# Kernel optimization log

Measured on AMD Instinct MI355X. Metric: run time of the kernel, lower is better.

The kernel has to match this reference:

```python
import jax, jax.numpy as jnp
import numpy as np
import math

D = 256        # input_size == d_k == d_v (per the module: d_k = input_size)
H = 4          # n_heads
MAX_LEN = 800  # PositionalEncoding max_len
NEG = float(-(2**32) + 1)
LN_EPS = 1e-5


def _make_pe():
    pe = np.zeros((MAX_LEN, D), dtype=np.float32)
    pos = np.arange(MAX_LEN, dtype=np.float32)[:, None]
    div = np.exp(np.arange(0, D, 2, dtype=np.float32) * -(math.log(10000.0) / D))
    pe[:, 0::2] = np.sin(pos * div)
    pe[:, 1::2] = np.cos(pos * div)
    return jnp.asarray(pe)


def setup_inputs() -> dict:
    key = jax.random.key(0)
    ks = jax.random.split(key, 12)
    B, L = 32, 512

    def xavier(k, shape):
        fan_in, fan_out = shape[0], shape[1]
        std = math.sqrt(2.0 / (fan_in + fan_out))
        return jax.random.normal(k, shape, dtype=jnp.float32) * std

    return {
        "Q": jax.random.normal(ks[0], (B, L, D), dtype=jnp.float32),
        "K": jax.random.normal(ks[1], (B, L, D), dtype=jnp.float32),
        "V": jax.random.normal(ks[2], (B, L, D), dtype=jnp.float32),
        "mask": jax.random.randint(ks[3], (B, L), 0, 2).astype(jnp.bool_),
        "pe": _make_pe(),
        "W_q": xavier(ks[4], (D, H * D)),
        "W_k": xavier(ks[5], (D, H * D)),
        "W_v": xavier(ks[6], (D, H * D)),
        "W_o": xavier(ks[7], (H * D, D)),
        "w1": xavier(ks[8], (D, D)),
        "b1": jnp.zeros((D,), dtype=jnp.float32),
        "w2": xavier(ks[9], (D, D)),
        "b2": jnp.zeros((D,), dtype=jnp.float32),
        "gamma": jnp.ones((D,), dtype=jnp.float32),
        "beta": jnp.zeros((D,), dtype=jnp.float32),
    }


def _layer_norm(x, gamma, beta):
    mu = jnp.mean(x, axis=-1, keepdims=True)
    var = jnp.mean(jnp.square(x - mu), axis=-1, keepdims=True)
    return (x - mu) * jax.lax.rsqrt(var + LN_EPS) * gamma + beta


def _mha(Q, K, V, mask, W_q, W_k, W_v, W_o):
    B, Lq, _ = Q.shape
    Lk = K.shape[1]

    def split_heads(X, W, L):
        # (B, L, D) @ (D, H*D) -> (B*H, L, D)
        return (X @ W).reshape(B, L, H, D).transpose(0, 2, 1, 3).reshape(B * H, L, D)

    Qh = split_heads(Q, W_q, Lq)
    Kh = split_heads(K, W_k, Lk)
    Vh = split_heads(V, W_v, Lk)

    scale = D ** 0.5 + 1e-6
    scores = jnp.einsum('bqd,bkd->bqk', Qh, Kh) / scale  # (B*H, Lq, Lk)

    pad = jnp.broadcast_to(mask[:, None, :], (B, H, Lq)).reshape(B * H, Lq)
    pad_mask = jnp.broadcast_to(pad[:, :, None], (B * H, Lq, Lk))
    causal = jnp.triu(jnp.ones((Lq, Lk), dtype=jnp.bool_), k=1)
    full_mask = causal[None] | pad_mask
    scores = jnp.where(full_mask, NEG, scores)

    att = jax.nn.softmax(scores, axis=-1)
    Vatt = jnp.einsum('bqk,bkd->bqd', att, Vh)  # (B*H, Lq, D)
    Vatt = Vatt.reshape(B, H, Lq, D).transpose(0, 2, 1, 3).reshape(B, Lq, H * D)
    return Vatt @ W_o


def reference(Q, K, V, mask, pe, W_q, W_k, W_v, W_o, w1, b1, w2, b2, gamma, beta):
    Lq, Lk, Lv = Q.shape[1], K.shape[1], V.shape[1]
    Qp = Q + pe[None, :Lq]
    Kp = K + pe[None, :Lk]
    Vp = V + pe[None, :Lv]

    Vatt = _mha(Qp, Kp, Vp, mask, W_q, W_k, W_v, W_o)
    X = _layer_norm(Qp + Vatt, gamma, beta)
    ffn = jax.nn.relu(X @ w1.T + b1) @ w2.T + b2
    return _layer_norm(ffn + X, gamma, beta)
```

## Files before the change

kernel.cpp:

```cpp
#include <hip/hip_runtime.h>
#include <stdint.h>

#define SEQ   512
#define DM    256
#define NB    32
#define NH    4
#define HD    (NH * DM)
#define PE_MASK (SEQ * DM - 1)
#define NEGV  (-4294967295.0f)

typedef __attribute__((ext_vector_type(8))) short short8;
typedef __attribute__((ext_vector_type(4))) float f32x4;

#if defined(__has_builtin)
#if __has_builtin(__builtin_amdgcn_global_load_lds)
#define HAS_ASYNC 1
#endif
#endif
#ifndef HAS_ASYNC
#define HAS_ASYNC 0
#endif

__device__ __forceinline__ float b2f(unsigned short u) {
    return __uint_as_float(((uint32_t)u) << 16);
}
__device__ __forceinline__ unsigned short f2b(float f) {
    uint32_t u = __float_as_uint(f);
    u += 0x7fffu + ((u >> 16) & 1u);
    return (unsigned short)(u >> 16);
}
__device__ __forceinline__ float fast_exp2(float x) {
    float r;
    asm("v_exp_f32 %0, %1" : "=v"(r) : "v"(x));
    return r;
}

__device__ __forceinline__ int swzb(int b) {
    return b ^ (((b >> 7) & 7) << 4);
}

__global__ __launch_bounds__(256) void prep_all(
    const unsigned char* __restrict__ mask_raw, int* __restrict__ maskc,
    const float* __restrict__ Wq, const float* __restrict__ Wk,
    const float* __restrict__ Wv, unsigned short* __restrict__ WqT,
    const float* __restrict__ Wo, unsigned short* __restrict__ WoT,
    const float* __restrict__ w1, const float* __restrict__ w2,
    unsigned short* __restrict__ o1, unsigned short* __restrict__ o2,
    const float* __restrict__ Q, const float* __restrict__ K,
    const float* __restrict__ V, const float* __restrict__ pe,
    unsigned short* __restrict__ Qp, unsigned short* __restrict__ Kp,
    unsigned short* __restrict__ Vp)
{
    __shared__ unsigned short tile[32][33];
    __shared__ int enc[2];
    const int blk = blockIdx.x;
    const int tid = threadIdx.x;

    if (blk < 64) {
        if (tid == 0) { enc[0] = 0; enc[1] = 0; }
        __syncthreads();
        if (tid < 255 && mask_raw[tid * 4 + 1]) atomicOr(&enc[0], 1);
        if (tid < 128 && ((const int*)mask_raw)[tid * 2 + 1]) atomicOr(&enc[1], 1);
        __syncthreads();
        int i = blk * 256 + tid;
        int v;
        if (enc[0])      v = (mask_raw[i] != 0);
        else if (enc[1]) v = (((const int*)mask_raw)[i] != 0);
        else             v = ((((const int*)mask_raw)[i * 2] |
                              ((const int*)mask_raw)[i * 2 + 1]) != 0);
        maskc[i] = v;
    } else if (blk < 832) {
        int t = blk - 64;
        int x = t & 31, y = (t >> 5) & 7, zz = t >> 8;
        const float* in = (zz == 0) ? Wq : (zz == 1) ? Wk : Wv;
        unsigned short* op = WqT + (long)zz * 262144;
        int r0 = y * 32, c0 = x * 32;
        int i = tid >> 3, j = (tid & 7) * 4;
        float4 v = *reinterpret_cast<const float4*>(in + (long)(r0 + i) * HD + c0 + j);
        tile[i][j + 0] = f2b(v.x); tile[i][j + 1] = f2b(v.y);
        tile[i][j + 2] = f2b(v.z); tile[i][j + 3] = f2b(v.w);
        __syncthreads();
        ushort4 w;
        w.x = tile[j + 0][i]; w.y = tile[j + 1][i];
        w.z = tile[j + 2][i]; w.w = tile[j + 3][i];
        *reinterpret_cast<ushort4*>(op + (long)(c0 + i) * DM + r0 + j) = w;
    } else if (blk < 1088) {
        int t = blk - 832;
        int x = t & 7, y = t >> 3;
        int r0 = y * 32, c0 = x * 32;
        int i = tid >> 3, j = (tid & 7) * 4;
        float4 v = *reinterpret_cast<const float4*>(Wo + (long)(r0 + i) * DM + c0 + j);
        tile[i][j + 0] = f2b(v.x); tile[i][j + 1] = f2b(v.y);
        tile[i][j + 2] = f2b(v.z); tile[i][j + 3] = f2b(v.w);
        __syncthreads();
        ushort4 w;
        w.x = tile[j + 0][i]; w.y = tile[j + 1][i];
        w.z = tile[j + 2][i]; w.w = tile[j + 3][i];
        *reinterpret_cast<ushort4*>(WoT + (long)(c0 + i) * HD + r0 + j) = w;
    } else if (blk < 1216) {
        int t = blk - 1088;
        const float* in = (t < 64) ? w1 : w2;
        unsigned short* out = (t < 64) ? o1 : o2;
        long i = (long)((t & 63) * 256 + tid) * 4;
        float4 x = *reinterpret_cast<const float4*>(in + i);
        ushort4 o;
        o.x = f2b(x.x); o.y = f2b(x.y); o.z = f2b(x.z); o.w = f2b(x.w);
        *reinterpret_cast<ushort4*>(out + i) = o;
    } else {
        int t = blk - 1216;
        int seg = t >> 12;
        const float* X = (seg == 0) ? Q : (seg == 1) ? K : V;
        unsigned short* O = (seg == 0) ? Qp : (seg == 1) ? Kp : Vp;
        long i = (long)((t & 4095) * 256 + tid) * 4;
        float4 x = *reinterpret_cast<const float4*>(X + i);
        float4 p = *reinterpret_cast<const float4*>(pe + (i & PE_MASK));
        ushort4 o;
        o.x = f2b(x.x + p.x); o.y = f2b(x.y + p.y);
        o.z = f2b(x.z + p.z); o.w = f2b(x.w + p.w);
        *reinterpret_cast<ushort4*>(O + i) = o;
    }
}

__global__ __launch_bounds__(256) void tv_kernel(
    const unsigned short* __restrict__ Vh, unsigned short* __restrict__ VhT,
    float* __restrict__ part, int nbl)
{
    __shared__ unsigned short tile[32][33];
    const int blk = blockIdx.x;
    const int tid = threadIdx.x;
    const int nT = nbl * NH * 128;

    if (blk < nT) {
        int x = blk & 7, y = (blk >> 3) & 15, zz = blk >> 7;
        int b = zz / NH, hh = zz % NH;
        const unsigned short* ip = Vh + (long)b * SEQ * HD + (long)hh * DM;
        unsigned short* op = VhT + (long)b * SEQ * HD + (long)hh * SEQ * DM;
        int r0 = y * 32, c0 = x * 32;
        int i = tid >> 3, j = (tid & 7) * 4;
        ushort4 v = *reinterpret_cast<const ushort4*>(ip + (long)(r0 + i) * HD + c0 + j);
        tile[i][j + 0] = v.x; tile[i][j + 1] = v.y;
        tile[i][j + 2] = v.z; tile[i][j + 3] = v.w;
        __syncthreads();
        ushort4 w;
        w.x = tile[j + 0][i]; w.y = tile[j + 1][i];
        w.z = tile[j + 2][i]; w.w = tile[j + 3][i];
        *reinterpret_cast<ushort4*>(op + (long)(c0 + i) * SEQ + r0 + j) = w;
    } else {
        int t = blk - nT;
        int bl = t >> 3, seg = t & 7;
        const unsigned short* p = Vh + (long)bl * SEQ * HD + (long)seg * 64 * HD;
        int c = tid * 4;
        float s0 = 0.f, s1 = 0.f, s2 = 0.f, s3 = 0.f;
        for (int l = 0; l < 64; ++l) {
            ushort4 v = *reinterpret_cast<const ushort4*>(p + (long)l * HD + c);
            s0 += b2f(v.x); s1 += b2f(v.y); s2 += b2f(v.z); s3 += b2f(v.w);
        }
        float4 o = {s0, s1, s2, s3};
        *reinterpret_cast<float4*>(part + (long)(bl * 8 + seg) * HD + c) = o;
    }
}

template<bool BIAS, bool RELU, bool OUTBF16>
__global__ __launch_bounds__(256) void gemm_bt(
    const unsigned short* __restrict__ A, int lda,
    const unsigned short* __restrict__ B, int ldb,
    void* __restrict__ Cv, int ldc,
    const float* __restrict__ bias, float scale, int K, int Hdiv,
    long sAb, long sAh, long sAz,
    long sBb, long sBh, long sBz,
    long sCb, long sCh, long sCz)
{
    const int m0 = blockIdx.y * 128;
    const int n0 = blockIdx.x * 128;
    int z  = blockIdx.z;
    int bb = z / Hdiv, hh = z % Hdiv;
    const unsigned short* Ab = A + bb * sAb + hh * sAh + (long)z * sAz;
    const unsigned short* Bb = B + bb * sBb + hh * sBh + (long)z * sBz;
    long coff = bb * sCb + hh * sCh + (long)z * sCz;
    const float scl = (z == 0) ? scale : 1.0f;

    __shared__ unsigned short As[2][128 * 32];
    __shared__ unsigned short Bs[2][128 * 32];

    const int tid  = threadIdx.x;
    const int lane = tid & 63;
    const int wave = tid >> 6;
    const int wm   = (wave >> 1) * 64;
    const int wn   = (wave & 1) * 64;
    const int lm   = lane & 15;
    const int kq   = (lane >> 4) * 8;

    f32x4 acc[4][4] = {};

    auto stage = [&](int b, int k0) {
#pragma unroll
        for (int it = 0; it < 2; ++it) {
            int id = tid + it * 256;
#if HAS_ASYNC
            int U  = swzb(id * 16);
            int r  = U >> 6;
            int c8 = ((U >> 4) & 3) * 8;
            const unsigned short* gA = Ab + (long)(m0 + r) * lda + k0 + c8;
            const unsigned short* gB = Bb + (long)(n0 + r) * ldb + k0 + c8;
            unsigned short* lA = &As[b][(size_t)(it * 256 + wave * 64) * 8];
            unsigned short* lB = &Bs[b][(size_t)(it * 256 + wave * 64) * 8];
            __builtin_amdgcn_global_load_lds(
                (const __attribute__((address_space(1))) void*)gA,
                (__attribute__((address_space(3))) void*)lA, 16, 0, 0);
            __builtin_amdgcn_global_load_lds(
                (const __attribute__((address_space(1))) void*)gB,
                (__attribute__((address_space(3))) void*)lB, 16, 0, 0);
#else
            int r  = id >> 2;
            int c8 = (id & 3) * 8;
            const unsigned short* gA = Ab + (long)(m0 + r) * lda + k0 + c8;
            const unsigned short* gB = Bb + (long)(n0 + r) * ldb + k0 + c8;
            *reinterpret_cast<uint4*>((char*)As[b] + swzb(id * 16)) =
                *reinterpret_cast<const uint4*>(gA);
            *reinterpret_cast<uint4*>((char*)Bs[b] + swzb(id * 16)) =
                *reinterpret_cast<const uint4*>(gB);
#endif
        }
    };

    stage(0, 0);
    __syncthreads();
    const int nk = K >> 5;
    for (int kk = 0; kk < nk; ++kk) {
        const int cur = kk & 1;
        if (kk + 1 < nk)
            stage(cur ^ 1, (kk + 1) * 32);

        short8 af[4], bfr[4];
#pragma unroll
        for (int i = 0; i < 4; ++i)
            af[i] = *reinterpret_cast<const short8*>(
                (const char*)As[cur] + swzb((wm + i * 16 + lm) * 64 + kq * 2));
#pragma unroll
        for (int j = 0; j < 4; ++j)
            bfr[j] = *reinterpret_cast<const short8*>(
                (const char*)Bs[cur] + swzb((wn + j * 16 + lm) * 64 + kq * 2));
#pragma unroll
        for (int i = 0; i < 4; ++i)
#pragma unroll
            for (int j = 0; j < 4; ++j)
                acc[i][j] = __builtin_amdgcn_mfma_f32_16x16x32_bf16(af[i], bfr[j], acc[i][j], 0, 0, 0);
        __syncthreads();
    }

#pragma unroll
    for (int j = 0; j < 4; ++j) {
        int col  = n0 + wn + j * 16 + lm;
        float bv = 0.f;
        if (BIAS) bv = bias[col];
#pragma unroll
        for (int i = 0; i < 4; ++i) {
#pragma unroll
            for (int r = 0; r < 4; ++r) {
                int row = m0 + wm + i * 16 + (lane >> 4) * 4 + r;
                float v = acc[i][j][r] * scl + bv;
                if (RELU) v = fmaxf(v, 0.f);
                long idx = coff + (long)row * ldc + col;
                if (OUTBF16) reinterpret_cast<unsigned short*>(Cv)[idx] = f2b(v);
                else         reinterpret_cast<float*>(Cv)[idx] = v;
            }
        }
    }
}

__device__ __forceinline__ void stage_k32(
    unsigned short* __restrict__ buf, const unsigned short* __restrict__ Ak,
    int kc, int qt, int tid, int wave)
{
    for (int it = 0; it <= qt; ++it) {
        int id = tid + it * 256;
#if HAS_ASYNC
        int U = swzb(id * 16);
        const unsigned short* g = Ak + (long)(U >> 6) * HD + kc * 32 + ((U >> 4) & 3) * 8;
        unsigned short* l = buf + (size_t)(it * 256 + wave * 64) * 8;
        __builtin_amdgcn_global_load_lds(
            (const __attribute__((address_space(1))) void*)g,
            (__attribute__((address_space(3))) void*)l, 16, 0, 0);
#else
        const unsigned short* g = Ak + (long)(id >> 2) * HD + kc * 32 + (id & 3) * 8;
        *reinterpret_cast<uint4*>((char*)buf + swzb(id * 16)) =
            *reinterpret_cast<const uint4*>(g);
#endif
    }
}

__device__ __forceinline__ void stage_v64(
    unsigned short* __restrict__ buf, const unsigned short* __restrict__ Av,
    int c64, int tid, int wave)
{
#pragma unroll
    for (int it = 0; it < 8; ++it) {
        int id = tid + it * 256;
#if HAS_ASYNC
        int U = swzb(id * 16);
        const unsigned short* g = Av + (long)(U >> 7) * SEQ + c64 * 64 + ((U >> 4) & 7) * 8;
        unsigned short* l = buf + (size_t)(it * 256 + wave * 64) * 8;
        __builtin_amdgcn_global_load_lds(
            (const __attribute__((address_space(1))) void*)g,
            (__attribute__((address_space(3))) void*)l, 16, 0, 0);
#else
        const unsigned short* g = Av + (long)(id >> 3) * SEQ + c64 * 64 + (id & 7) * 8;
        *reinterpret_cast<uint4*>((char*)buf + swzb(id * 16)) =
            *reinterpret_cast<const uint4*>(g);
#endif
    }
}

__global__ __launch_bounds__(256, 2) void flash_attn(
    const unsigned short* __restrict__ Qh,
    const unsigned short* __restrict__ Kh,
    const unsigned short* __restrict__ VhT,
    const float* __restrict__ part,
    unsigned short* __restrict__ Vatt,
    const int* __restrict__ maskc, int bh0, int nbh)
{
    const int tid  = threadIdx.x;
    const int lane = tid & 63;
    const int wave = tid >> 6;
    const int lm   = lane & 15;
    const int qg   = lane >> 4;
    const int kq   = qg * 8;

    const int L = blockIdx.x;
    int z, qt;
    if ((nbh & 7) == 0) {
        int x = L & 7, m = L >> 3;
        int mq = m & 7;
        qt = (mq & 1) ? (7 - (mq >> 1)) : (mq >> 1);
        z  = x + 8 * (m >> 3);
    } else {
        z = L % nbh; qt = L / nbh;
    }
    const int b_l = z >> 2, h = z & 3;
    const int m0  = qt * 64;
    const int wq0 = m0 + wave * 16;
    const long qkbase = (long)b_l * SEQ * HD + (long)h * DM;
    const unsigned short* Aq = Qh + qkbase;
    const unsigned short* Ak = Kh + qkbase;
    const unsigned short* Av = VhT + (long)b_l * SEQ * HD + (long)h * SEQ * DM;
    unsigned short* Ov = Vatt + qkbase;
    const int bglob = (bh0 + z) >> 2;

    __shared__ unsigned short Ks[2 * SEQ * 32];
    __shared__ __align__(16) unsigned short Pw[4][16][40];

    f32x4 S[32] = {};
    const int NT = (m0 >> 4) + wave + 1;

    stage_k32(Ks, Ak, 0, qt, tid, wave);
    __syncthreads();
    for (int kc = 0; kc < 8; ++kc) {
        unsigned short* cur = (kc & 1) ? (Ks + SEQ * 32) : Ks;
        unsigned short* nxt = (kc & 1) ? Ks : (Ks + SEQ * 32);
        short8 qf = *reinterpret_cast<const short8*>(
            Aq + (long)(wq0 + lm) * HD + kc * 32 + kq);
        if (kc < 7) {
            stage_k32(nxt, Ak, kc + 1, qt, tid, wave);
        } else {
            stage_v64(Ks, Av, 0, tid, wave);
        }
        __builtin_amdgcn_s_setprio(1);
#pragma unroll
        for (int nt = 0; nt < 32; ++nt) {
            if (nt < NT) {
                int row = nt * 16 + lm;
                short8 bf = *reinterpret_cast<const short8*>(
                    (const char*)cur + swzb(row * 64 + qg * 16));
                S[nt] = __builtin_amdgcn_mfma_f32_16x16x32_bf16(qf, bf, S[nt], 0, 0, 0);
            }
        }
        __builtin_amdgcn_s_setprio(0);
        __syncthreads();
    }

    int   qrow[4];
    bool  rowm[4];
    float mx[4], sm[4];
#pragma unroll
    for (int r = 0; r < 4; ++r) {
        int q = wq0 + qg * 4 + r;
        qrow[r] = q;
        rowm[r] = maskc[bglob * SEQ + q] != 0;
        mx[r] = -3.4e38f;
    }
#pragma unroll
    for (int nt = 0; nt < 32; ++nt) {
        int k = nt * 16 + lm;
#pragma unroll
        for (int r = 0; r < 4; ++r) {
            float v = S[nt][r];
            if (k > qrow[r]) v = NEGV;
            S[nt][r] = v;
            mx[r] = fmaxf(mx[r], v);
        }
    }
#pragma unroll
    for (int r = 0; r < 4; ++r) {
#pragma unroll
        for (int off = 8; off >= 1; off >>= 1)
            mx[r] = fmaxf(mx[r], __shfl_xor(mx[r], off));
        sm[r] = 0.f;
    }
    uint32_t pk[32][2];
#pragma unroll
    for (int nt = 0; nt < 32; ++nt) {
        float e0 = fast_exp2(S[nt][0] - mx[0]);
        float e1 = fast_exp2(S[nt][1] - mx[1]);
        float e2 = fast_exp2(S[nt][2] - mx[2]);
        float e3 = fast_exp2(S[nt][3] - mx[3]);
        sm[0] += e0; sm[1] += e1; sm[2] += e2; sm[3] += e3;
        pk[nt][0] = (uint32_t)f2b(e0) | ((uint32_t)f2b(e1) << 16);
        pk[nt][1] = (uint32_t)f2b(e2) | ((uint32_t)f2b(e3) << 16);
    }
#pragma unroll
    for (int r = 0; r < 4; ++r) {
#pragma unroll
        for (int off = 8; off >= 1; off >>= 1)
            sm[r] += __shfl_xor(sm[r], off);
        sm[r] = 1.0f / sm[r];
    }

    unsigned short* Vb0 = Ks;
    unsigned short* Vb1 = Ks + 16384;
    const int NC = qt + 1;
    f32x4 O[16] = {};
#pragma unroll
    for (int c64 = 0; c64 < 8; ++c64) {
        if (c64 < NC) {
            unsigned short* Vcur = (c64 & 1) ? Vb1 : Vb0;
            __syncthreads();
            if (c64 + 1 < NC) {
                unsigned short* Vnext = (c64 & 1) ? Vb0 : Vb1;
                stage_v64(Vnext, Av, c64 + 1, tid, wave);
            }
#pragma unroll
            for (int t = 0; t < 2; ++t) {
#pragma unroll
                for (int tt = 0; tt < 2; ++tt) {
                    int nt = c64 * 4 + t * 2 + tt;
#pragma unroll
                    for (int r = 0; r < 4; ++r)
                        Pw[wave][qg * 4 + r][tt * 16 + lm] =
                            (unsigned short)(pk[nt][r >> 1] >> ((r & 1) * 16));
                }
                short8 pf = *reinterpret_cast<const short8*>(&Pw[wave][lm][kq]);
                __builtin_amdgcn_s_setprio(1);
#pragma unroll
                for (int nt2 = 0; nt2 < 16; ++nt2) {
                    int row = nt2 * 16 + lm;
                    short8 vf = *reinterpret_cast<const short8*>(
                        (const char*)Vcur + swzb(row * 128 + t * 64 + qg * 16));
                    O[nt2] = __builtin_amdgcn_mfma_f32_16x16x32_bf16(pf, vf, O[nt2], 0, 0, 0);
                }
                __builtin_amdgcn_s_setprio(0);
            }
        }
    }

    const float* pb = part + (long)(b_l * 8) * HD + h * DM + lm;
    float vmf[16];
#pragma unroll
    for (int nt2 = 0; nt2 < 16; ++nt2) {
        float s = 0.f;
#pragma unroll
        for (int seg = 0; seg < 8; ++seg)
            s += pb[(long)seg * HD + nt2 * 16];
        vmf[nt2] = s * (1.0f / SEQ);
    }
#pragma unroll
    for (int nt2 = 0; nt2 < 16; ++nt2) {
#pragma unroll
        for (int r = 0; r < 4; ++r) {
            int l = wq0 + qg * 4 + r;
            float val = rowm[r] ? vmf[nt2] : O[nt2][r] * sm[r];
            Ov[(long)l * HD + nt2 * 16 + lm] = f2b(val);
        }
    }
}

__global__ __launch_bounds__(256) void ln1_kernel(
    const unsigned short* __restrict__ AttO, const float* __restrict__ Q,
    const float* __restrict__ pe,
    const float* __restrict__ gamma, const float* __restrict__ beta,
    float* __restrict__ outf, unsigned short* __restrict__ outb)
{
    int row  = blockIdx.x * 4 + (threadIdx.x >> 6);
    int lane = threadIdx.x & 63;
    long base = (long)row * DM + lane * 4;
    ushort4 a = *reinterpret_cast<const ushort4*>(AttO + base);
    float4 qv = *reinterpret_cast<const float4*>(Q + base);
    float4 pv = *reinterpret_cast<const float4*>(pe + (base & PE_MASK));
    float x[4] = {b2f(a.x) + qv.x + pv.x, b2f(a.y) + qv.y + pv.y,
                  b2f(a.z) + qv.z + pv.z, b2f(a.w) + qv.w + pv.w};
    float s = x[0] + x[1] + x[2] + x[3];
#pragma unroll
    for (int off = 32; off > 0; off >>= 1) s += __shfl_xor(s, off);
    float mu = s * (1.0f / DM);
    float vs = 0.f;
#pragma unroll
    for (int t = 0; t < 4; ++t) { float d = x[t] - mu; vs += d * d; }
#pragma unroll
    for (int off = 32; off > 0; off >>= 1) vs += __shfl_xor(vs, off);
    float inv = rsqrtf(vs * (1.0f / DM) + 1e-5f);
    int d0 = lane * 4;
    float4 g = *reinterpret_cast<const float4*>(gamma + d0);
    float4 bt = *reinterpret_cast<const float4*>(beta + d0);
    float4 o;
    o.x = (x[0] - mu) * inv * g.x + bt.x;
    o.y = (x[1] - mu) * inv * g.y + bt.y;
    o.z = (x[2] - mu) * inv * g.z + bt.z;
    o.w = (x[3] - mu) * inv * g.w + bt.w;
    *reinterpret_cast<float4*>(outf + base) = o;
    ushort4 ob;
    ob.x = f2b(o.x); ob.y = f2b(o.y); ob.z = f2b(o.z); ob.w = f2b(o.w);
    *reinterpret_cast<ushort4*>(outb + base) = ob;
}

__global__ __launch_bounds__(256) void ln2_kernel(
    const float* __restrict__ F, const float* __restrict__ X,
    const float* __restrict__ gamma, const float* __restrict__ beta,
    float* __restrict__ out)
{
    int row  = blockIdx.x * 4 + (threadIdx.x >> 6);
    int lane = threadIdx.x & 63;
    long base = (long)row * DM + lane * 4;
    float4 a = *reinterpret_cast<const float4*>(F + base);
    float4 c = *reinterpret_cast<const float4*>(X + base);
    float x[4] = {a.x + c.x, a.y + c.y, a.z + c.z, a.w + c.w};
    float s = x[0] + x[1] + x[2] + x[3];
#pragma unroll
    for (int off = 32; off > 0; off >>= 1) s += __shfl_xor(s, off);
    float mu = s * (1.0f / DM);
    float vs = 0.f;
#pragma unroll
    for (int t = 0; t < 4; ++t) { float d = x[t] - mu; vs += d * d; }
#pragma unroll
    for (int off = 32; off > 0; off >>= 1) vs += __shfl_xor(vs, off);
    float inv = rsqrtf(vs * (1.0f / DM) + 1e-5f);
    int d0 = lane * 4;
    float4 g = *reinterpret_cast<const float4*>(gamma + d0);
    float4 bt = *reinterpret_cast<const float4*>(beta + d0);
    float4 o;
    o.x = (x[0] - mu) * inv * g.x + bt.x;
    o.y = (x[1] - mu) * inv * g.y + bt.y;
    o.z = (x[2] - mu) * inv * g.z + bt.z;
    o.w = (x[3] - mu) * inv * g.w + bt.w;
    *reinterpret_cast<float4*>(out + base) = o;
}

extern "C" void kernel_launch(void* const* d_in, const int* in_sizes, int n_in,
                              void* d_out, int out_size, void* d_ws, size_t ws_size,
                              hipStream_t stream)
{
    const float* Q  = (const float*)d_in[0];
    const float* Ki = (const float*)d_in[1];
    const float* Vi = (const float*)d_in[2];
    const unsigned char* mask_raw = (const unsigned char*)d_in[3];
    const float* pe = (const float*)d_in[4];
    const float* Wq = (const float*)d_in[5];
    const float* Wk = (const float*)d_in[6];
    const float* Wv = (const float*)d_in[7];
    const float* Wo = (const float*)d_in[8];
    const float* w1 = (const float*)d_in[9];
    const float* b1 = (const float*)d_in[10];
    const float* w2 = (const float*)d_in[11];
    const float* b2 = (const float*)d_in[12];
    const float* gamma = (const float*)d_in[13];
    const float* beta  = (const float*)d_in[14];
    float* out = (float*)d_out;

    const size_t MiB = 1048576;
    char* ws = (char*)d_ws;

    int CB = 1;
    for (int cb = 32; cb >= 1; cb >>= 1) {
        size_t scr_sz = (size_t)(5 * cb) * MiB + (size_t)cb * 32768;
        if (scr_sz < 24 * MiB) scr_sz = 24 * MiB;
        if ((59 * MiB + scr_sz) <= ws_size) { CB = cb; break; }
    }
    const int NCH = NB / CB;

    unsigned short* WqT  = (unsigned short*)(ws);
    unsigned short* WkT  = WqT + 262144;
    unsigned short* WvT  = WkT + 262144;
    unsigned short* WoT  = WvT + 262144;
    unsigned short* w1b  = (unsigned short*)(ws + 2 * MiB);
    unsigned short* w2b  = w1b + 65536;
    int*            maskc = (int*)(ws + 2 * MiB + 262144);
    unsigned short* Qp   = (unsigned short*)(ws + 3 * MiB);
    unsigned short* Kp   = (unsigned short*)(ws + 11 * MiB);
    unsigned short* Vp   = (unsigned short*)(ws + 19 * MiB);
    unsigned short* AttO = (unsigned short*)(ws + 27 * MiB);
    unsigned short* Xb   = (unsigned short*)(ws + 35 * MiB);
    float*          Xf   = (float*)(ws + 43 * MiB);
    char*           scr  = ws + 59 * MiB;
    unsigned short* Qh   = (unsigned short*)(scr);
    unsigned short* Kh   = (unsigned short*)(scr + (size_t)CB * MiB);
    unsigned short* Vh   = (unsigned short*)(scr + (size_t)2 * CB * MiB);
    unsigned short* VhT  = (unsigned short*)(scr + (size_t)3 * CB * MiB);
    unsigned short* Vatt = (unsigned short*)(scr + (size_t)4 * CB * MiB);
    float*          part = (float*)(scr + (size_t)5 * CB * MiB);
    unsigned short* H1   = (unsigned short*)(scr);
    float*          Ff   = (float*)(scr + 8 * MiB);

    const float SCALE_Q = (float)((1.0 / (16.0 + 1e-6)) * 1.4426950408889634);
    const long CROWS = (long)CB * SEQ;
    const long CBELT = (long)CB * MiB / 2;

    prep_all<<<13504, 256, 0, stream>>>(
        mask_raw, maskc, Wq, Wk, Wv, WqT, Wo, WoT,
        w1, w2, w1b, w2b, Q, Ki, Vi, pe, Qp, Kp, Vp);

    for (int c = 0; c < NCH; ++c) {
        const long r0   = (long)c * CROWS;
        const int  bh0  = c * CB * NH;
        const int  gy   = (int)(CROWS / 128);
        const int  nbh  = CB * NH;

        gemm_bt<false, false, true><<<dim3(8, gy, 3), 256, 0, stream>>>(
            Qp + r0 * DM, DM, WqT, DM, Qh, HD, nullptr, SCALE_Q, DM,
            1, 4194304, 0, 0, 262144, 0, 0, CBELT, 0, 0);

        tv_kernel<<<CB * NH * 128 + CB * 8, 256, 0, stream>>>(
            Vh, VhT, part, CB);

        flash_attn<<<dim3(8 * nbh, 1, 1), 256, 0, stream>>>(
            Qh, Kh, VhT, part, Vatt, maskc, bh0, nbh);

        gemm_bt<false, false, true><<<dim3(2, gy, 1), 256, 0, stream>>>(
            Vatt, HD, WoT, HD, AttO + r0 * DM, DM, nullptr, 1.f, HD,
            1, 0,0,0, 0,0,0, 0,0,0);
    }

    ln1_kernel<<<4096, 256, 0, stream>>>(AttO, Q, pe, gamma, beta, Xf, Xb);

    gemm_bt<true, true, true><<<dim3(2, 128, 1), 256, 0, stream>>>(
        Xb, DM, w1b, DM, H1, DM, b1, 1.f, DM, 1, 0,0,0, 0,0,0, 0,0,0);
    gemm_bt<true, false, false><<<dim3(2, 128, 1), 256, 0, stream>>>(
        H1, DM, w2b, DM, Ff, DM, b2, 1.f, DM, 1, 0,0,0, 0,0,0, 0,0,0);

    ln2_kernel<<<4096, 256, 0, stream>>>(Ff, Xf, gamma, beta, out);
}
```

Before: 324.7 us.

## Fuse output-projection and FFN2 GEMMs with residual layernorm epilogues

Adds a gemm_ln kernel in which each block computes a full 64x256 output row tile and applies the residual add, optional positional encoding and bias, and layernorm in the epilogue through an LDS staging tile. It replaces the W_o GEMM plus ln1 and the second FFN GEMM plus ln2, removing the intermediate AttO and Ff buffers and two extra launches. In exchange each block must own the whole 256-wide row, so fewer blocks run (for example 256 for FFN2), which lowers parallelism and uses a large LDS tile that may reduce occupancy.

```diff
diff --git a/kernel.cpp b/kernel.cpp
--- a/kernel.cpp
+++ b/kernel.cpp
@@ -268,6 +268,155 @@
     }
 }
 
+template<bool ADDPE, bool BIAS, bool OUTB16>
+__global__ __launch_bounds__(256) void gemm_ln(
+    const unsigned short* __restrict__ A, int lda,
+    const unsigned short* __restrict__ B, int ldb,
+    const float* __restrict__ bias,
+    const float* __restrict__ Rf, const float* __restrict__ pe,
+    const float* __restrict__ gamma, const float* __restrict__ beta,
+    float* __restrict__ outf, unsigned short* __restrict__ outb,
+    int K, long row0)
+{
+    const int m0 = blockIdx.x * 64;
+
+    __shared__ __align__(16) float Xt[64][260];
+    unsigned short* Sh = reinterpret_cast<unsigned short*>(&Xt[0][0]);
+    unsigned short* AsP[2] = { Sh, Sh + 2048 };
+    unsigned short* BsP[2] = { Sh + 4096, Sh + 4096 + 8192 };
+
+    const int tid  = threadIdx.x;
+    const int lane = tid & 63;
+    const int wave = tid >> 6;
+    const int wm   = (wave >> 1) * 32;
+    const int wn   = (wave & 1) * 128;
+    const int lm   = lane & 15;
+    const int qg   = lane >> 4;
+    const int kq   = qg * 8;
+
+    f32x4 acc[2][8] = {};
+
+    auto stage = [&](int b, int k0) {
+        {
+            int id = tid;
+#if HAS_ASYNC
+            int U  = swzb(id * 16);
+            int r  = U >> 6;
+            int c8 = ((U >> 4) & 3) * 8;
+            const unsigned short* gA = A + (long)(m0 + r) * lda + k0 + c8;
+            unsigned short* lA = AsP[b] + (size_t)(wave * 64) * 8;
+            __builtin_amdgcn_global_load_lds(
+                (const __attribute__((address_space(1))) void*)gA,
+                (__attribute__((address_space(3))) void*)lA, 16, 0, 0);
+#else
+            int r  = id >> 2;
+            int c8 = (id & 3) * 8;
+            const unsigned short* gA = A + (long)(m0 + r) * lda + k0 + c8;
+            *reinterpret_cast<uint4*>((char*)AsP[b] + swzb(id * 16)) =
+                *reinterpret_cast<const uint4*>(gA);
+#endif
+        }
+#pragma unroll
+        for (int it = 0; it < 4; ++it) {
+            int id = tid + it * 256;
+#if HAS_ASYNC
+            int U  = swzb(id * 16);
+            int r  = U >> 6;
+            int c8 = ((U >> 4) & 3) * 8;
+            const unsigned short* gB = B + (long)r * ldb + k0 + c8;
+            unsigned short* lB = BsP[b] + (size_t)(it * 256 + wave * 64) * 8;
+            __builtin_amdgcn_global_load_lds(
+                (const __attribute__((address_space(1))) void*)gB,
+                (__attribute__((address_space(3))) void*)lB, 16, 0, 0);
+#else
+            int r  = id >> 2;
+            int c8 = (id & 3) * 8;
+            const unsigned short* gB = B + (long)r * ldb + k0 + c8;
+            *reinterpret_cast<uint4*>((char*)BsP[b] + swzb(id * 16)) =
+                *reinterpret_cast<const uint4*>(gB);
+#endif
+        }
+    };
+
+    stage(0, 0);
+    __syncthreads();
+    const int nk = K >> 5;
+    for (int kk = 0; kk < nk; ++kk) {
+        const int cur = kk & 1;
+        if (kk + 1 < nk)
+            stage(cur ^ 1, (kk + 1) * 32);
+
+        short8 af[2], bfr[8];
+#pragma unroll
+        for (int i = 0; i < 2; ++i)
+            af[i] = *reinterpret_cast<const short8*>(
+                (const char*)AsP[cur] + swzb((wm + i * 16 + lm) * 64 + kq * 2));
+#pragma unroll
+        for (int j = 0; j < 8; ++j)
+            bfr[j] = *reinterpret_cast<const short8*>(
+                (const char*)BsP[cur] + swzb((wn + j * 16 + lm) * 64 + kq * 2));
+#pragma unroll
+        for (int i = 0; i < 2; ++i)
+#pragma unroll
+            for (int j = 0; j < 8; ++j)
+                acc[i][j] = __builtin_amdgcn_mfma_f32_16x16x32_bf16(af[i], bfr[j], acc[i][j], 0, 0, 0);
+        __syncthreads();
+    }
+
+#pragma unroll
+    for (int j = 0; j < 8; ++j) {
+        int col = wn + j * 16 + lm;
+#pragma unroll
+        for (int i = 0; i < 2; ++i)
+#pragma unroll
+            for (int r = 0; r < 4; ++r)
+                Xt[wm + i * 16 + qg * 4 + r][col] = acc[i][j][r];
+    }
+    __syncthreads();
+
+    for (int rr = 0; rr < 16; ++rr) {
+        int lrow = rr * 4 + (tid >> 6);
+        long grow = row0 + m0 + lrow;
+        long base = grow * DM + lane * 4;
+        int d0 = lane * 4;
+        float4 xv = *reinterpret_cast<const float4*>(&Xt[lrow][d0]);
+        float x[4] = {xv.x, xv.y, xv.z, xv.w};
+        if (BIAS) {
+            float4 bv = *reinterpret_cast<const float4*>(bias + d0);
+            x[0] += bv.x; x[1] += bv.y; x[2] += bv.z; x[3] += bv.w;
+        }
+        float4 rv = *reinterpret_cast<const float4*>(Rf + base);
+        x[0] += rv.x; x[1] += rv.y; x[2] += rv.z; x[3] += rv.w;
+        if (ADDPE) {
+            float4 pv = *reinterpret_cast<const float4*>(pe + (base & PE_MASK));
+            x[0] += pv.x; x[1] += pv.y; x[2] += pv.z; x[3] += pv.w;
+        }
+        float s = x[0] + x[1] + x[2] + x[3];
+#pragma unroll
+        for (int off = 32; off > 0; off >>= 1) s += __shfl_xor(s, off);
+        float mu = s * (1.0f / DM);
+        float vs = 0.f;
+#pragma unroll
+        for (int t = 0; t < 4; ++t) { float d = x[t] - mu; vs += d * d; }
+#pragma unroll
+        for (int off = 32; off > 0; off >>= 1) vs += __shfl_xor(vs, off);
+        float inv = rsqrtf(vs * (1.0f / DM) + 1e-5f);
+        float4 g  = *reinterpret_cast<const float4*>(gamma + d0);
+        float4 bt = *reinterpret_cast<const float4*>(beta + d0);
+        float4 o;
+        o.x = (x[0] - mu) * inv * g.x + bt.x;
+        o.y = (x[1] - mu) * inv * g.y + bt.y;
+        o.z = (x[2] - mu) * inv * g.z + bt.z;
+        o.w = (x[3] - mu) * inv * g.w + bt.w;
+        *reinterpret_cast<float4*>(outf + base) = o;
+        if (OUTB16) {
+            ushort4 ob;
+            ob.x = f2b(o.x); ob.y = f2b(o.y); ob.z = f2b(o.z); ob.w = f2b(o.w);
+            *reinterpret_cast<ushort4*>(outb + base) = ob;
+        }
+    }
+}
+
 __device__ __forceinline__ void stage_k32(
     unsigned short* __restrict__ buf, const unsigned short* __restrict__ Ak,
     int kc, int qt, int tid, int wave)
@@ -481,76 +630,6 @@
             Ov[(long)l * HD + nt2 * 16 + lm] = f2b(val);
         }
     }
-}
-
-__global__ __launch_bounds__(256) void ln1_kernel(
-    const unsigned short* __restrict__ AttO, const float* __restrict__ Q,
-    const float* __restrict__ pe,
-    const float* __restrict__ gamma, const float* __restrict__ beta,
-    float* __restrict__ outf, unsigned short* __restrict__ outb)
-{
-    int row  = blockIdx.x * 4 + (threadIdx.x >> 6);
-    int lane = threadIdx.x & 63;
-    long base = (long)row * DM + lane * 4;
-    ushort4 a = *reinterpret_cast<const ushort4*>(AttO + base);
-    float4 qv = *reinterpret_cast<const float4*>(Q + base);
-    float4 pv = *reinterpret_cast<const float4*>(pe + (base & PE_MASK));
-    float x[4] = {b2f(a.x) + qv.x + pv.x, b2f(a.y) + qv.y + pv.y,
-                  b2f(a.z) + qv.z + pv.z, b2f(a.w) + qv.w + pv.w};
-    float s = x[0] + x[1] + x[2] + x[3];
-#pragma unroll
-    for (int off = 32; off > 0; off >>= 1) s += __shfl_xor(s, off);
-    float mu = s * (1.0f / DM);
-    float vs = 0.f;
-#pragma unroll
-    for (int t = 0; t < 4; ++t) { float d = x[t] - mu; vs += d * d; }
-#pragma unroll
-    for (int off = 32; off > 0; off >>= 1) vs += __shfl_xor(vs, off);
-    float inv = rsqrtf(vs * (1.0f / DM) + 1e-5f);
-    int d0 = lane * 4;
-    float4 g = *reinterpret_cast<const float4*>(gamma + d0);
-    float4 bt = *reinterpret_cast<const float4*>(beta + d0);
-    float4 o;
-    o.x = (x[0] - mu) * inv * g.x + bt.x;
-    o.y = (x[1] - mu) * inv * g.y + bt.y;
-    o.z = (x[2] - mu) * inv * g.z + bt.z;
-    o.w = (x[3] - mu) * inv * g.w + bt.w;
-    *reinterpret_cast<float4*>(outf + base) = o;
-    ushort4 ob;
-    ob.x = f2b(o.x); ob.y = f2b(o.y); ob.z = f2b(o.z); ob.w = f2b(o.w);
-    *reinterpret_cast<ushort4*>(outb + base) = ob;
-}
-
-__global__ __launch_bounds__(256) void ln2_kernel(
-    const float* __restrict__ F, const float* __restrict__ X,
-    const float* __restrict__ gamma, const float* __restrict__ beta,
-    float* __restrict__ out)
-{
-    int row  = blockIdx.x * 4 + (threadIdx.x >> 6);
-    int lane = threadIdx.x & 63;
-    long base = (long)row * DM + lane * 4;
-    float4 a = *reinterpret_cast<const float4*>(F + base);
-    float4 c = *reinterpret_cast<const float4*>(X + base);
-    float x[4] = {a.x + c.x, a.y + c.y, a.z + c.z, a.w + c.w};
-    float s = x[0] + x[1] + x[2] + x[3];
-#pragma unroll
-    for (int off = 32; off > 0; off >>= 1) s += __shfl_xor(s, off);
-    float mu = s * (1.0f / DM);
-    float vs = 0.f;
-#pragma unroll
-    for (int t = 0; t < 4; ++t) { float d = x[t] - mu; vs += d * d; }
-#pragma unroll
-    for (int off = 32; off > 0; off >>= 1) vs += __shfl_xor(vs, off);
-    float inv = rsqrtf(vs * (1.0f / DM) + 1e-5f);
-    int d0 = lane * 4;
-    float4 g = *reinterpret_cast<const float4*>(gamma + d0);
-    float4 bt = *reinterpret_cast<const float4*>(beta + d0);
-    float4 o;
-    o.x = (x[0] - mu) * inv * g.x + bt.x;
-    o.y = (x[1] - mu) * inv * g.y + bt.y;
-    o.z = (x[2] - mu) * inv * g.z + bt.z;
-    o.w = (x[3] - mu) * inv * g.w + bt.w;
-    *reinterpret_cast<float4*>(out + base) = o;
 }
 
 extern "C" void kernel_launch(void* const* d_in, const int* in_sizes, int n_in,
@@ -595,7 +674,6 @@
     unsigned short* Qp   = (unsigned short*)(ws + 3 * MiB);
     unsigned short* Kp   = (unsigned short*)(ws + 11 * MiB);
     unsigned short* Vp   = (unsigned short*)(ws + 19 * MiB);
-    unsigned short* AttO = (unsigned short*)(ws + 27 * MiB);
     unsigned short* Xb   = (unsigned short*)(ws + 35 * MiB);
     float*          Xf   = (float*)(ws + 43 * MiB);
     char*           scr  = ws + 59 * MiB;
@@ -606,7 +684,6 @@
     unsigned short* Vatt = (unsigned short*)(scr + (size_t)4 * CB * MiB);
     float*          part = (float*)(scr + (size_t)5 * CB * MiB);
     unsigned short* H1   = (unsigned short*)(scr);
-    float*          Ff   = (float*)(scr + 8 * MiB);
 
     const float SCALE_Q = (float)((1.0 / (16.0 + 1e-6)) * 1.4426950408889634);
     const long CROWS = (long)CB * SEQ;
@@ -632,17 +709,15 @@
         flash_attn<<<dim3(8 * nbh, 1, 1), 256, 0, stream>>>(
             Qh, Kh, VhT, part, Vatt, maskc, bh0, nbh);
 
-        gemm_bt<false, false, true><<<dim3(2, gy, 1), 256, 0, stream>>>(
-            Vatt, HD, WoT, HD, AttO + r0 * DM, DM, nullptr, 1.f, HD,
-            1, 0,0,0, 0,0,0, 0,0,0);
-    }
-
-    ln1_kernel<<<4096, 256, 0, stream>>>(AttO, Q, pe, gamma, beta, Xf, Xb);
+        gemm_ln<true, false, true><<<(int)(CROWS / 64), 256, 0, stream>>>(
+            Vatt, HD, WoT, HD, nullptr, Q, pe, gamma, beta,
+            Xf, Xb, HD, r0);
+    }
 
     gemm_bt<true, true, true><<<dim3(2, 128, 1), 256, 0, stream>>>(
         Xb, DM, w1b, DM, H1, DM, b1, 1.f, DM, 1, 0,0,0, 0,0,0, 0,0,0);
-    gemm_bt<true, false, false><<<dim3(2, 128, 1), 256, 0, stream>>>(
-        H1, DM, w2b, DM, Ff, DM, b2, 1.f, DM, 1, 0,0,0, 0,0,0, 0,0,0);
-
-    ln2_kernel<<<4096, 256, 0, stream>>>(Ff, Xf, gamma, beta, out);
-}
+
+    gemm_ln<false, true, false><<<256, 256, 0, stream>>>(
+        H1, DM, w2b, DM, b2, Xf, nullptr, gamma, beta,
+        out, nullptr, DM, 0);
+}
```

New measurement: 333.4 us. +2.7%, slower.
